# Performance work log

Measured on AMD Instinct MI355X. Metric: run time of the kernel, lower is better.

## Reference

```python
import jax, jax.numpy as jnp
import numpy as np

B, N, M = 2, 2048, 128
H, D = 16, 64
IN_DIM, CTX_DIM = 1024, 768


def layernorm(x, g, b, eps=1e-5):
    mu = x.mean(-1, keepdims=True)
    var = ((x - mu) ** 2).mean(-1, keepdims=True)
    return (x - mu) * jax.lax.rsqrt(var + eps) * g + b


def setup_inputs() -> dict:
    key = jax.random.key(0)
    ks = jax.random.split(key, 8)
    w = lambda i, sh: jax.random.normal(ks[i], sh, jnp.float32) * 0.02
    return {
        "x": jax.random.normal(ks[0], (B, N, IN_DIM), jnp.float32),
        "c_emb": jax.random.normal(ks[1], (B, M, CTX_DIM), jnp.float32),
        "ln_g": jnp.ones((IN_DIM,), jnp.float32),
        "ln_b": jnp.zeros((IN_DIM,), jnp.float32),
        "ctx_ln_g": jnp.ones((CTX_DIM,), jnp.float32),
        "ctx_ln_b": jnp.zeros((CTX_DIM,), jnp.float32),
        "W_ctx": w(2, (CTX_DIM, 2 * D)),
        "b_ctx": jnp.zeros((2 * D,), jnp.float32),
        "W_q": w(3, (IN_DIM, H * D)),
        "W_kv": w(4, (IN_DIM, 2 * H * D)),
        "null_kv": jax.random.normal(ks[5], (2, D), jnp.float32),
        "W_out": w(6, (H * D, IN_DIM)),
        "out_ln_g": jnp.ones((IN_DIM,), jnp.float32),
        "out_ln_b": jnp.zeros((IN_DIM,), jnp.float32),
    }


def reference(x, c_emb, ln_g, ln_b, ctx_ln_g, ctx_ln_b, W_ctx, b_ctx,
              W_q, W_kv, null_kv, W_out, out_ln_g, out_ln_b):
    b, n, _ = x.shape
    xn = layernorm(x, ln_g, ln_b)
    q = (xn @ W_q).reshape(b, n, H, D)                      # [b,n,h,d]
    kv = (xn @ W_kv).reshape(b, n, 2, H, D)
    k, v = kv[:, :, 0], kv[:, :, 1]                         # [b,n,h,d]
    # context projected to a single shared-across-heads k and v
    ckv = layernorm(c_emb, ctx_ln_g, ctx_ln_b) @ W_ctx + b_ctx
    ck, cv = jnp.split(ckv, 2, axis=-1)                     # [b,m,d]
    nk = jnp.broadcast_to(null_kv[0], (b, 1, D))
    nv = jnp.broadcast_to(null_kv[1], (b, 1, D))
    k_ext = jnp.concatenate([nk, ck], axis=1)               # [b,m+1,d]
    v_ext = jnp.concatenate([nv, cv], axis=1)
    scale = D ** -0.5
    s_self = jnp.einsum('bnhd,bkhd->bhnk', q, k) * scale    # [b,h,n,n]
    s_ctx = jnp.einsum('bnhd,bkd->bhnk', q, k_ext) * scale  # [b,h,n,m+1]
    w = jax.nn.softmax(jnp.concatenate([s_self, s_ctx], axis=-1), axis=-1)
    w_self, w_ctx = w[..., :n], w[..., n:]
    out = (jnp.einsum('bhnk,bkhd->bnhd', w_self, v)
           + jnp.einsum('bhnk,bkd->bnhd', w_ctx, v_ext))    # [b,n,h,d]
    out = out.reshape(b, n, H * D) @ W_out                  # [b,n,input_dim]
    return layernorm(out, out_ln_g, out_ln_b)
```

## Files before the change

kernel.cpp:

```cpp
#include <hip/hip_runtime.h>
#include <cstdint>
#include <cstddef>

typedef __attribute__((ext_vector_type(8))) short bf16x8;
typedef __attribute__((ext_vector_type(4))) short bf16x4;
typedef __attribute__((ext_vector_type(4))) float f32x4;
typedef __attribute__((ext_vector_type(4))) unsigned int u32x4;
typedef __attribute__((ext_vector_type(2))) unsigned int u32x2;

__device__ inline unsigned short f2b(float f){
  unsigned int u = __float_as_uint(f);
  u += 0x7fffu + ((u >> 16) & 1u);
  return (unsigned short)(u >> 16);
}
__device__ inline unsigned int pk2(float a, float b){
  unsigned int ua = __float_as_uint(a) + 0x8000u;
  unsigned int ub = __float_as_uint(b) + 0x8000u;
  return __builtin_amdgcn_perm(ub, ua, 0x07060302u);
}
__device__ inline void gl2lds16(const void* g, void* l){
  __builtin_amdgcn_global_load_lds(
      (const __attribute__((address_space(1))) unsigned int*)g,
      (__attribute__((address_space(3))) unsigned int*)l, 16, 0, 0);
}

#define QSCALE 0.18033688011112042f

__global__ __launch_bounds__(256) void wcvt_kernel(
    const float* __restrict__ Wq, const float* __restrict__ Wkv,
    const float* __restrict__ Wout,
    unsigned short* __restrict__ Wqkv_t, unsigned short* __restrict__ Wout_t)
{
  __shared__ short tile[64*72];
  int cg0 = blockIdx.x * 64;
  int kt  = blockIdx.y * 64;
  const float* src; int ld; int col0; unsigned short* dst; int drow0;
  if (cg0 < 1024)      { src = Wq;   ld = 1024; col0 = cg0;        dst = Wqkv_t; drow0 = cg0; }
  else if (cg0 < 3072) { src = Wkv;  ld = 2048; col0 = cg0 - 1024; dst = Wqkv_t; drow0 = cg0; }
  else                 { src = Wout; ld = 1024; col0 = cg0 - 3072; dst = Wout_t; drow0 = cg0 - 3072; }
  int t = threadIdx.x;
  #pragma unroll
  for (int i = 0; i < 16; ++i){
    int lin = t + 256*i;
    int k = lin >> 6, c = lin & 63;
    tile[k*72 + c] = (short)f2b(src[(size_t)(kt + k)*ld + col0 + c]);
  }
  __syncthreads();
  #pragma unroll
  for (int i = 0; i < 16; ++i){
    int lin = t + 256*i;
    int c = lin >> 6, k = lin & 63;
    dst[(size_t)(drow0 + c)*1024 + kt + k] = (unsigned short)tile[k*72 + c];
  }
}

template<bool BF16OUT>
__global__ __launch_bounds__(256) void ln1024_kernel(
    const float* __restrict__ X, const float* __restrict__ G,
    const float* __restrict__ Bb, void* __restrict__ out)
{
  int row = blockIdx.x, t = threadIdx.x;
  float4 x = ((const float4*)(X + (size_t)row*1024))[t];
  float s  = x.x + x.y + x.z + x.w;
  float s2 = x.x*x.x + x.y*x.y + x.z*x.z + x.w*x.w;
  #pragma unroll
  for (int o = 32; o > 0; o >>= 1){ s += __shfl_down(s, o); s2 += __shfl_down(s2, o); }
  __shared__ float red[8];
  int w = t >> 6;
  if ((t & 63) == 0){ red[w] = s; red[4 + w] = s2; }
  __syncthreads();
  float mu  = (red[0]+red[1]+red[2]+red[3]) * (1.0f/1024.0f);
  float var = (red[4]+red[5]+red[6]+red[7]) * (1.0f/1024.0f) - mu*mu;
  float rstd = rsqrtf(var + 1e-5f);
  float4 g = ((const float4*)G)[t];
  float4 b = ((const float4*)Bb)[t];
  float y0 = (x.x-mu)*rstd*g.x + b.x;
  float y1 = (x.y-mu)*rstd*g.y + b.y;
  float y2 = (x.z-mu)*rstd*g.z + b.z;
  float y3 = (x.w-mu)*rstd*g.w + b.w;
  if (BF16OUT){
    ushort4 u; u.x = f2b(y0); u.y = f2b(y1); u.z = f2b(y2); u.w = f2b(y3);
    ((ushort4*)out)[(size_t)row*256 + t] = u;
  } else {
    float4 y; y.x = y0; y.y = y1; y.z = y2; y.w = y3;
    ((float4*)out)[(size_t)row*256 + t] = y;
  }
}

__global__ __launch_bounds__(128) void ctx_kernel(
    const float* __restrict__ Cemb, const float* __restrict__ G,
    const float* __restrict__ Bb, const float* __restrict__ Wctx,
    const float* __restrict__ bctx, const float* __restrict__ nullkv,
    unsigned short* __restrict__ kext, unsigned short* __restrict__ vext_t)
{
  int row = blockIdx.x;
  int b = row >> 7, m = row & 127;
  int t = threadIdx.x;
  if (row < 128){
    int b2 = row >> 6, fr = row & 63;
    int frow = (fr == 0) ? 0 : (128 + fr);
    if (t < 64){
      kext[((size_t)b2*192 + frow)*64 + t] = (frow == 0) ? f2b(nullkv[t]) : (unsigned short)0;
    } else {
      int d = t - 64;
      vext_t[((size_t)b2*64 + d)*192 + frow] = (frow == 0) ? f2b(nullkv[64 + d]) : (unsigned short)0;
    }
  }
  const float* xr = Cemb + (size_t)row*768;
  float v[6]; float s = 0.f, s2 = 0.f;
  #pragma unroll
  for (int j = 0; j < 6; ++j){ float xv = xr[t + 128*j]; v[j] = xv; s += xv; s2 += xv*xv; }
  #pragma unroll
  for (int o = 32; o > 0; o >>= 1){ s += __shfl_down(s, o); s2 += __shfl_down(s2, o); }
  __shared__ float red[4];
  __shared__ float xn[768];
  int w = t >> 6;
  if ((t & 63) == 0){ red[w] = s; red[2 + w] = s2; }
  __syncthreads();
  float mu  = (red[0]+red[1]) * (1.0f/768.0f);
  float var = (red[2]+red[3]) * (1.0f/768.0f) - mu*mu;
  float rstd = rsqrtf(var + 1e-5f);
  #pragma unroll
  for (int j = 0; j < 6; ++j){ int c = t + 128*j; xn[c] = (v[j]-mu)*rstd*G[c] + Bb[c]; }
  __syncthreads();
  float acc = bctx[t];
  #pragma unroll 8
  for (int j = 0; j < 768; ++j) acc += xn[j] * Wctx[j*128 + t];
  unsigned short hv = f2b(acc);
  if (t < 64) kext[((size_t)b*192 + 1 + m)*64 + t] = hv;
  else        vext_t[((size_t)b*64 + (t - 64))*192 + 1 + m] = hv;
}

#define GEMM_MAINLOOP(A_, Bt_, tM_, tN_)                                        \
  __shared__ __align__(16) short sA[128*64];                                    \
  __shared__ __align__(16) short sB[128*64];                                    \
  int t = threadIdx.x, w = t >> 6, lane = t & 63;                               \
  int wm = w & 1, wn = w >> 1, lm = lane & 15, q = lane >> 4;                   \
  int grow = lane >> 3;                                                         \
  int gchk = ((lane & 7) ^ grow) << 3;                                          \
  f32x4 acc[4][4] = {};                                                         \
  const unsigned short* Aw = A_ + (size_t)(tM_ + w*32 + grow)*1024 + gchk;      \
  const unsigned short* Bw = Bt_ + (size_t)(tN_ + w*32 + grow)*1024 + gchk;     \
  for (int kk = 0; kk < 1024; kk += 64){                                        \
    __syncthreads();                                                            \
    gl2lds16(Aw + kk,            &sA[(w*32     )*64]);                          \
    gl2lds16(Aw + kk +  8*1024,  &sA[(w*32 +  8)*64]);                          \
    gl2lds16(Aw + kk + 16*1024,  &sA[(w*32 + 16)*64]);                          \
    gl2lds16(Aw + kk + 24*1024,  &sA[(w*32 + 24)*64]);                          \
    gl2lds16(Bw + kk,            &sB[(w*32     )*64]);                          \
    gl2lds16(Bw + kk +  8*1024,  &sB[(w*32 +  8)*64]);                          \
    gl2lds16(Bw + kk + 16*1024,  &sB[(w*32 + 16)*64]);                          \
    gl2lds16(Bw + kk + 24*1024,  &sB[(w*32 + 24)*64]);                          \
    __syncthreads();                                                            \
    bf16x8 af[4][2], bfr[4][2];                                                 \
    _Pragma("unroll")                                                           \
    for (int i = 0; i < 4; ++i){                                                \
      int ra = wm*64 + i*16 + lm, rb = wn*64 + i*16 + lm;                       \
      _Pragma("unroll")                                                         \
      for (int hh = 0; hh < 2; ++hh){                                           \
        int sw = ((hh*4 + q) ^ (lm & 7)) << 3;                                  \
        af[i][hh]  = *(const bf16x8*)(&sA[ra*64 + sw]);                         \
        bfr[i][hh] = *(const bf16x8*)(&sB[rb*64 + sw]);                         \
      }                                                                         \
    }                                                                           \
    _Pragma("unroll")                                                           \
    for (int hh = 0; hh < 2; ++hh)                                              \
      _Pragma("unroll")                                                         \
      for (int i = 0; i < 4; ++i)                                               \
        _Pragma("unroll")                                                       \
        for (int j = 0; j < 4; ++j)                                             \
          acc[i][j] = __builtin_amdgcn_mfma_f32_16x16x32_bf16(af[i][hh], bfr[j][hh], acc[i][j], 0, 0, 0); \
  }

__global__ __launch_bounds__(256) void gemm_qkv_kernel(
    const unsigned short* __restrict__ A, const unsigned short* __restrict__ Bt,
    unsigned short* __restrict__ Qb, unsigned short* __restrict__ Kb,
    unsigned short* __restrict__ VtG)
{
  int id = blockIdx.x;
  int xcd = id & 7, r = id >> 3;
  int tM = ((r & 3)*8 + xcd) * 128;
  int tN = (r >> 2) * 128;
  GEMM_MAINLOOP(A, Bt, tM, tN)
  if (tN < 1024){
    #pragma unroll
    for (int i = 0; i < 4; ++i){
      int R0 = tM + wm*64 + i*16 + q*4;
      int b = R0 >> 11, n = R0 & 2047;
      #pragma unroll
      for (int j = 0; j < 4; ++j){
        int Cg = tN + wn*64 + j*16 + lm;
        int h = Cg >> 6, d = Cg & 63;
        size_t base = ((((size_t)(b*16 + h) << 11) | n) << 6) + d;
        #pragma unroll
        for (int rr = 0; rr < 4; ++rr)
          Qb[base + (size_t)rr*64] = f2b(acc[i][j][rr] * QSCALE);
      }
    }
  } else if (tN < 2048){
    #pragma unroll
    for (int i = 0; i < 4; ++i){
      int R0 = tM + wm*64 + i*16 + q*4;
      int b = R0 >> 11, n = R0 & 2047;
      #pragma unroll
      for (int j = 0; j < 4; ++j){
        int c2 = tN - 1024 + wn*64 + j*16 + lm;
        int h = c2 >> 6, d = c2 & 63;
        size_t base = ((((size_t)(b*16 + h) << 11) | n) << 6) + d;
        #pragma unroll
        for (int rr = 0; rr < 4; ++rr)
          Kb[base + (size_t)rr*64] = f2b(acc[i][j][rr]);
      }
    }
  } else {
    #pragma unroll
    for (int i = 0; i < 4; ++i){
      int R0 = tM + wm*64 + i*16 + q*4;
      int b = R0 >> 11, n = R0 & 2047;
      #pragma unroll
      for (int j = 0; j < 4; ++j){
        int c2 = tN - 2048 + wn*64 + j*16 + lm;
        int h = c2 >> 6, d = c2 & 63;
        ushort4 u;
        u.x = f2b(acc[i][j][0]); u.y = f2b(acc[i][j][1]);
        u.z = f2b(acc[i][j][2]); u.w = f2b(acc[i][j][3]);
        *(ushort4*)(VtG + ((size_t)(b*16 + h)*64 + d)*2048 + n) = u;
      }
    }
  }
}

__global__ __launch_bounds__(256) void gemm_out_kernel(
    const unsigned short* __restrict__ A, const unsigned short* __restrict__ Bt,
    float* __restrict__ C)
{
  int id = blockIdx.x;
  int xcd = id & 7, r = id >> 3;
  int tM = ((r & 3)*8 + xcd) * 128;
  int tN = (r >> 2) * 128;
  GEMM_MAINLOOP(A, Bt, tM, tN)
  #pragma unroll
  for (int i = 0; i < 4; ++i){
    int R0 = tM + wm*64 + i*16 + q*4;
    #pragma unroll
    for (int j = 0; j < 4; ++j){
      int Cg = tN + wn*64 + j*16 + lm;
      #pragma unroll
      for (int rr = 0; rr < 4; ++rr)
        C[(size_t)(R0 + rr)*1024 + Cg] = acc[i][j][rr];
    }
  }
}

__global__ __launch_bounds__(512, 2) void attn_kernel(
    const unsigned short* __restrict__ Qb, const unsigned short* __restrict__ Kb,
    const unsigned short* __restrict__ VtG, const unsigned short* __restrict__ kext,
    const unsigned short* __restrict__ vext_t, unsigned short* __restrict__ Ob)
{
  __shared__ __align__(16) char smem[81920];
  int id = blockIdx.x;
  int xcd = id & 7, slot = id >> 3;
  int bh = xcd*4 + (slot >> 4);
  int qt = slot & 15;
  int b = bh >> 4, h = bh & 15;
  int t = threadIdx.x, w = t >> 6, lane = t & 63;
  int p = w >> 1, lw = w & 1;
  int lm = lane & 15, q = lane >> 4;
  int esw = lm & 7;

  short* myK = (short*)(smem + p*8192);
  short* myV = (short*)(smem + 32768 + p*8192);
  short* pw  = (short*)(smem + 65536 + w*2048);

  const unsigned short* Qbase = Qb + ((size_t)bh*2048 + qt*128 + lw*64)*64;
  bf16x8 qf[4][2];
  #pragma unroll
  for (int qq = 0; qq < 4; ++qq){
    qf[qq][0] = *(const bf16x8*)(Qbase + (size_t)(qq*16 + lm)*64 + q*8);
    qf[qq][1] = *(const bf16x8*)(Qbase + (size_t)(qq*16 + lm)*64 + q*8 + 32);
  }

  f32x4 o[4][4] = {};
  float l_i[4] = {0.f, 0.f, 0.f, 0.f};

  int pt = t & 127;
  int r0 = pt >> 1, c0 = (pt & 1) << 5;
  int rsw = r0 & 7;
  const int t0 = p*9;
  const int t1 = (p == 3) ? 35 : (t0 + 9);

  u32x4 kr[4], vr[4];
  {
    const unsigned short* kp = Kb + ((size_t)bh*2048 + t0*64 + r0)*64 + c0;
    const unsigned short* vp = VtG + ((size_t)bh*64 + r0)*2048 + t0*64 + c0;
    #pragma unroll
    for (int jj = 0; jj < 4; ++jj){
      kr[jj] = *(const u32x4*)(kp + 8*jj);
      vr[jj] = *(const u32x4*)(vp + 8*jj);
    }
  }

  for (int it = 0; it < 9; ++it){
    int tile = t0 + it;
    bool valid = tile < t1;
    __syncthreads();
    if (valid){
      #pragma unroll
      for (int jj = 0; jj < 4; ++jj){
        int gsw = ((((pt & 1) << 2) | jj) ^ rsw) << 3;
        *(u32x4*)(&myK[r0*64 + gsw]) = kr[jj];
        *(u32x4*)(&myV[r0*64 + gsw]) = vr[jj];
      }
    }
    __syncthreads();

    int nt = tile + 1;
    if (nt < t1){
      bool ext = nt >= 32;
      int kb = ext ? (nt - 32)*64 : nt*64;
      const unsigned short* kp = ext ? (kext + ((size_t)b*192 + kb + r0)*64 + c0)
                                     : (Kb + ((size_t)bh*2048 + kb + r0)*64 + c0);
      const unsigned short* vp = ext ? (vext_t + ((size_t)b*64 + r0)*192 + kb + c0)
                                     : (VtG + ((size_t)bh*64 + r0)*2048 + kb + c0);
      #pragma unroll
      for (int jj = 0; jj < 4; ++jj){
        kr[jj] = *(const u32x4*)(kp + 8*jj);
        vr[jj] = *(const u32x4*)(vp + 8*jj);
      }
    }
    if (!valid) continue;

    bf16x8 kf[4][2];
    #pragma unroll
    for (int st = 0; st < 4; ++st){
      kf[st][0] = *(const bf16x8*)(&myK[(st*16 + lm)*64 + ((q       ^ esw) << 3)]);
      kf[st][1] = *(const bf16x8*)(&myK[(st*16 + lm)*64 + (((4 + q) ^ esw) << 3)]);
    }

    #pragma unroll
    for (int qp = 0; qp < 2; ++qp){
      f32x4 s[2][4];
      #pragma unroll
      for (int qh = 0; qh < 2; ++qh){
        int qq = qp*2 + qh;
        #pragma unroll
        for (int st = 0; st < 4; ++st){
          f32x4 z = {};
          z = __builtin_amdgcn_mfma_f32_16x16x32_bf16(kf[st][0], qf[qq][0], z, 0, 0, 0);
          s[qh][st] = __builtin_amdgcn_mfma_f32_16x16x32_bf16(kf[st][1], qf[qq][1], z, 0, 0, 0);
        }
      }
      if (tile == 34){
        #pragma unroll
        for (int qh = 0; qh < 2; ++qh)
          #pragma unroll
          for (int st = 0; st < 4; ++st)
            #pragma unroll
            for (int rr = 0; rr < 4; ++rr){
              int key = 128 + st*16 + q*4 + rr;
              if (key >= 129) s[qh][st][rr] = -1e30f;
            }
      }
      bf16x8 pb[2][2];
      #pragma unroll
      for (int qh = 0; qh < 2; ++qh){
        float sm = 0.f;
        #pragma unroll
        for (int st = 0; st < 4; ++st)
          #pragma unroll
          for (int rr = 0; rr < 4; ++rr){
            float pv = __builtin_amdgcn_exp2f(s[qh][st][rr]);
            s[qh][st][rr] = pv; sm += pv;
          }
        l_i[qp*2 + qh] += sm;
        #pragma unroll
        for (int st = 0; st < 4; ++st){
          u32x2 pkd;
          pkd[0] = pk2(s[qh][st][0], s[qh][st][1]);
          pkd[1] = pk2(s[qh][st][2], s[qh][st][3]);
          int gsw = ((((st << 1) | (q >> 1)) ^ esw) << 3) + ((q & 1) << 2);
          *(u32x2*)(&pw[lm*64 + gsw]) = pkd;
        }
        bf16x4 a0 = *(const bf16x4*)(&pw[lm*64 + ((q       ^ esw) << 3)]);
        bf16x4 a1 = *(const bf16x4*)(&pw[lm*64 + ((q       ^ esw) << 3) + 4]);
        bf16x4 a2 = *(const bf16x4*)(&pw[lm*64 + (((4 + q) ^ esw) << 3)]);
        bf16x4 a3 = *(const bf16x4*)(&pw[lm*64 + (((4 + q) ^ esw) << 3) + 4]);
        pb[qh][0] = __builtin_shufflevector(a0, a1, 0,1,2,3,4,5,6,7);
        pb[qh][1] = __builtin_shufflevector(a2, a3, 0,1,2,3,4,5,6,7);
      }
      #pragma unroll
      for (int ds = 0; ds < 4; ++ds){
        bf16x8 af0 = *(const bf16x8*)(&myV[(ds*16 + lm)*64 + ((q       ^ esw) << 3)]);
        bf16x8 af1 = *(const bf16x8*)(&myV[(ds*16 + lm)*64 + (((4 + q) ^ esw) << 3)]);
        #pragma unroll
        for (int qh = 0; qh < 2; ++qh){
          int qq = qp*2 + qh;
          o[ds][qq] = __builtin_amdgcn_mfma_f32_16x16x32_bf16(af0, pb[qh][0], o[ds][qq], 0, 0, 0);
          o[ds][qq] = __builtin_amdgcn_mfma_f32_16x16x32_bf16(af1, pb[qh][1], o[ds][qq], 0, 0, 0);
        }
      }
    }
  }

  float* mb = (float*)smem;
  float* lb = (float*)(smem + 65536);
  int ms = ((p >> 1) << 1) | lw;
  float* reg = mb + ms*4096 + lane*64;
  float* lr  = lb + ms*256 + lane*4;
  int fsw = lane & 15;
  __syncthreads();
  if (p & 1){
    #pragma unroll
    for (int ds = 0; ds < 4; ++ds)
      #pragma unroll
      for (int qq = 0; qq < 4; ++qq)
        *(f32x4*)(reg + (((ds*4 + qq) ^ fsw) << 2)) = o[ds][qq];
    #pragma unroll
    for (int qq = 0; qq < 4; ++qq) lr[qq] = l_i[qq];
  }
  __syncthreads();
  if (!(p & 1)){
    #pragma unroll
    for (int ds = 0; ds < 4; ++ds)
      #pragma unroll
      for (int qq = 0; qq < 4; ++qq)
        o[ds][qq] += *(const f32x4*)(reg + (((ds*4 + qq) ^ fsw) << 2));
    #pragma unroll
    for (int qq = 0; qq < 4; ++qq) l_i[qq] += lr[qq];
    if (p == 2){
      #pragma unroll
      for (int ds = 0; ds < 4; ++ds)
        #pragma unroll
        for (int qq = 0; qq < 4; ++qq)
          *(f32x4*)(reg + (((ds*4 + qq) ^ fsw) << 2)) = o[ds][qq];
      #pragma unroll
      for (int qq = 0; qq < 4; ++qq) lr[qq] = l_i[qq];
    }
  }
  __syncthreads();
  if (p == 0){
    float* reg2 = mb + (2 | lw)*4096 + lane*64;
    float* lr2  = lb + (2 | lw)*256 + lane*4;
    #pragma unroll
    for (int qq = 0; qq < 4; ++qq){
      #pragma unroll
      for (int ds = 0; ds < 4; ++ds){
        f32x4 ov = *(const f32x4*)(reg2 + (((ds*4 + qq) ^ fsw) << 2));
        o[ds][qq] += ov;
      }
      float l = l_i[qq] + lr2[qq];
      l += __shfl_xor(l, 16);
      l += __shfl_xor(l, 32);
      float inv = 1.0f / l;
      int n = qt*128 + lw*64 + qq*16 + lm;
      size_t base = ((size_t)b*2048 + n)*1024 + h*64 + q*4;
      #pragma unroll
      for (int ds = 0; ds < 4; ++ds){
        ushort4 u;
        u.x = f2b(o[ds][qq][0] * inv); u.y = f2b(o[ds][qq][1] * inv);
        u.z = f2b(o[ds][qq][2] * inv); u.w = f2b(o[ds][qq][3] * inv);
        *(ushort4*)(Ob + base + ds*16) = u;
      }
    }
  }
}

extern "C" void kernel_launch(void* const* d_in, const int* in_sizes, int n_in,
                              void* d_out, int out_size, void* d_ws, size_t ws_size,
                              hipStream_t stream)
{
  const float* x       = (const float*)d_in[0];
  const float* c_emb   = (const float*)d_in[1];
  const float* ln_g    = (const float*)d_in[2];
  const float* ln_b    = (const float*)d_in[3];
  const float* ctx_g   = (const float*)d_in[4];
  const float* ctx_b   = (const float*)d_in[5];
  const float* W_ctx   = (const float*)d_in[6];
  const float* b_ctx   = (const float*)d_in[7];
  const float* W_q     = (const float*)d_in[8];
  const float* W_kv    = (const float*)d_in[9];
  const float* null_kv = (const float*)d_in[10];
  const float* W_out   = (const float*)d_in[11];
  const float* oln_g   = (const float*)d_in[12];
  const float* oln_b   = (const float*)d_in[13];
  float* out = (float*)d_out;

  char* p = (char*)d_ws;
  unsigned short* xn     = (unsigned short*)p; p += (size_t)4096*1024*2;
  unsigned short* Wqkv_t = (unsigned short*)p; p += (size_t)3072*1024*2;
  unsigned short* Wout_t = (unsigned short*)p; p += (size_t)1024*1024*2;
  unsigned short* Qb     = (unsigned short*)p; p += (size_t)32*2048*64*2;
  unsigned short* Kb     = (unsigned short*)p; p += (size_t)32*2048*64*2;
  unsigned short* VtG    = (unsigned short*)p; p += (size_t)32*64*2048*2;
  unsigned short* kext   = (unsigned short*)p; p += (size_t)2*192*64*2;
  unsigned short* vext_t = (unsigned short*)p; p += (size_t)2*64*192*2;
  unsigned short* aout   = (unsigned short*)p; p += (size_t)4096*1024*2;
  float*          ptmp   = (float*)p;          p += (size_t)4096*1024*4;

  wcvt_kernel<<<dim3(64,16), 256, 0, stream>>>(W_q, W_kv, W_out, Wqkv_t, Wout_t);
  ln1024_kernel<true><<<4096, 256, 0, stream>>>(x, ln_g, ln_b, (void*)xn);
  ctx_kernel<<<256, 128, 0, stream>>>(c_emb, ctx_g, ctx_b, W_ctx, b_ctx, null_kv, kext, vext_t);
  gemm_qkv_kernel<<<768, 256, 0, stream>>>(xn, Wqkv_t, Qb, Kb, VtG);
  attn_kernel<<<512, 512, 0, stream>>>(Qb, Kb, VtG, kext, vext_t, aout);
  gemm_out_kernel<<<256, 256, 0, stream>>>(aout, Wout_t, ptmp);
  ln1024_kernel<false><<<4096, 256, 0, stream>>>(ptmp, oln_g, oln_b, (void*)out);
}
```

Before: 275.9 us.

## Load K/V fragments directly from global memory in attention, drop LDS staging

The attention kernel no longer stages K and V tiles through shared memory with register prefetch and barriers. Each wave now reads its MFMA operand fragments straight from global memory, relying on the caches. Blocks shrink from 512 to 256 threads, each handling 64 queries, with twice as many blocks and less shared memory per block. This removes the per-tile barriers and LDS copies but adds uncached-pattern global loads and duplicates K/V reads across more blocks.

```diff
diff --git a/kernel.cpp b/kernel.cpp
--- a/kernel.cpp
+++ b/kernel.cpp
@@ -252,27 +252,24 @@
   }
 }
 
-__global__ __launch_bounds__(512, 2) void attn_kernel(
+__global__ __launch_bounds__(256, 4) void attn_kernel(
     const unsigned short* __restrict__ Qb, const unsigned short* __restrict__ Kb,
     const unsigned short* __restrict__ VtG, const unsigned short* __restrict__ kext,
     const unsigned short* __restrict__ vext_t, unsigned short* __restrict__ Ob)
 {
-  __shared__ __align__(16) char smem[81920];
+  __shared__ __align__(16) char smem[36864];
   int id = blockIdx.x;
-  int xcd = id & 7, slot = id >> 3;
-  int bh = xcd*4 + (slot >> 4);
-  int qt = slot & 15;
+  int xcd = id & 7, s = id >> 3;
+  int bh = xcd*4 + (s >> 5);
+  int q64 = s & 31;
   int b = bh >> 4, h = bh & 15;
   int t = threadIdx.x, w = t >> 6, lane = t & 63;
-  int p = w >> 1, lw = w & 1;
   int lm = lane & 15, q = lane >> 4;
   int esw = lm & 7;
 
-  short* myK = (short*)(smem + p*8192);
-  short* myV = (short*)(smem + 32768 + p*8192);
-  short* pw  = (short*)(smem + 65536 + w*2048);
-
-  const unsigned short* Qbase = Qb + ((size_t)bh*2048 + qt*128 + lw*64)*64;
+  short* pw = (short*)(smem + w*2048);
+
+  const unsigned short* Qbase = Qb + ((size_t)bh*2048 + q64*64)*64;
   bf16x8 qf[4][2];
   #pragma unroll
   for (int qq = 0; qq < 4; ++qq){
@@ -283,63 +280,29 @@
   f32x4 o[4][4] = {};
   float l_i[4] = {0.f, 0.f, 0.f, 0.f};
 
-  int pt = t & 127;
-  int r0 = pt >> 1, c0 = (pt & 1) << 5;
-  int rsw = r0 & 7;
-  const int t0 = p*9;
-  const int t1 = (p == 3) ? 35 : (t0 + 9);
-
-  u32x4 kr[4], vr[4];
-  {
-    const unsigned short* kp = Kb + ((size_t)bh*2048 + t0*64 + r0)*64 + c0;
-    const unsigned short* vp = VtG + ((size_t)bh*64 + r0)*2048 + t0*64 + c0;
-    #pragma unroll
-    for (int jj = 0; jj < 4; ++jj){
-      kr[jj] = *(const u32x4*)(kp + 8*jj);
-      vr[jj] = *(const u32x4*)(vp + 8*jj);
-    }
-  }
-
-  for (int it = 0; it < 9; ++it){
-    int tile = t0 + it;
-    bool valid = tile < t1;
-    __syncthreads();
-    if (valid){
-      #pragma unroll
-      for (int jj = 0; jj < 4; ++jj){
-        int gsw = ((((pt & 1) << 2) | jj) ^ rsw) << 3;
-        *(u32x4*)(&myK[r0*64 + gsw]) = kr[jj];
-        *(u32x4*)(&myV[r0*64 + gsw]) = vr[jj];
-      }
-    }
-    __syncthreads();
-
-    int nt = tile + 1;
-    if (nt < t1){
-      bool ext = nt >= 32;
-      int kb = ext ? (nt - 32)*64 : nt*64;
-      const unsigned short* kp = ext ? (kext + ((size_t)b*192 + kb + r0)*64 + c0)
-                                     : (Kb + ((size_t)bh*2048 + kb + r0)*64 + c0);
-      const unsigned short* vp = ext ? (vext_t + ((size_t)b*64 + r0)*192 + kb + c0)
-                                     : (VtG + ((size_t)bh*64 + r0)*2048 + kb + c0);
-      #pragma unroll
-      for (int jj = 0; jj < 4; ++jj){
-        kr[jj] = *(const u32x4*)(kp + 8*jj);
-        vr[jj] = *(const u32x4*)(vp + 8*jj);
-      }
-    }
-    if (!valid) continue;
-
+  const int t0 = w*9;
+  const int t1 = (w == 3) ? 35 : (t0 + 9);
+
+  for (int tile = t0; tile < t1; ++tile){
+    bool ext = tile >= 32;
+    const unsigned short* kp = ext
+        ? kext + ((size_t)b*192 + (tile - 32)*64)*64
+        : Kb   + ((size_t)bh*2048 + tile*64)*64;
     bf16x8 kf[4][2];
     #pragma unroll
     for (int st = 0; st < 4; ++st){
-      kf[st][0] = *(const bf16x8*)(&myK[(st*16 + lm)*64 + ((q       ^ esw) << 3)]);
-      kf[st][1] = *(const bf16x8*)(&myK[(st*16 + lm)*64 + (((4 + q) ^ esw) << 3)]);
-    }
+      const unsigned short* kr = kp + (size_t)(st*16 + lm)*64 + q*8;
+      kf[st][0] = *(const bf16x8*)(kr);
+      kf[st][1] = *(const bf16x8*)(kr + 32);
+    }
+    const unsigned short* vp = ext
+        ? vext_t + (size_t)b*64*192 + (tile - 32)*64
+        : VtG    + (size_t)bh*64*2048 + tile*64;
+    size_t vstride = ext ? 192 : 2048;
 
     #pragma unroll
     for (int qp = 0; qp < 2; ++qp){
-      f32x4 s[2][4];
+      f32x4 sc[2][4];
       #pragma unroll
       for (int qh = 0; qh < 2; ++qh){
         int qq = qp*2 + qh;
@@ -347,7 +310,7 @@
         for (int st = 0; st < 4; ++st){
           f32x4 z = {};
           z = __builtin_amdgcn_mfma_f32_16x16x32_bf16(kf[st][0], qf[qq][0], z, 0, 0, 0);
-          s[qh][st] = __builtin_amdgcn_mfma_f32_16x16x32_bf16(kf[st][1], qf[qq][1], z, 0, 0, 0);
+          sc[qh][st] = __builtin_amdgcn_mfma_f32_16x16x32_bf16(kf[st][1], qf[qq][1], z, 0, 0, 0);
         }
       }
       if (tile == 34){
@@ -358,7 +321,7 @@
             #pragma unroll
             for (int rr = 0; rr < 4; ++rr){
               int key = 128 + st*16 + q*4 + rr;
-              if (key >= 129) s[qh][st][rr] = -1e30f;
+              if (key >= 129) sc[qh][st][rr] = -1e30f;
             }
       }
       bf16x8 pb[2][2];
@@ -369,15 +332,15 @@
         for (int st = 0; st < 4; ++st)
           #pragma unroll
           for (int rr = 0; rr < 4; ++rr){
-            float pv = __builtin_amdgcn_exp2f(s[qh][st][rr]);
-            s[qh][st][rr] = pv; sm += pv;
+            float pv = __builtin_amdgcn_exp2f(sc[qh][st][rr]);
+            sc[qh][st][rr] = pv; sm += pv;
           }
         l_i[qp*2 + qh] += sm;
         #pragma unroll
         for (int st = 0; st < 4; ++st){
           u32x2 pkd;
-          pkd[0] = pk2(s[qh][st][0], s[qh][st][1]);
-          pkd[1] = pk2(s[qh][st][2], s[qh][st][3]);
+          pkd[0] = pk2(sc[qh][st][0], sc[qh][st][1]);
+          pkd[1] = pk2(sc[qh][st][2], sc[qh][st][3]);
           int gsw = ((((st << 1) | (q >> 1)) ^ esw) << 3) + ((q & 1) << 2);
           *(u32x2*)(&pw[lm*64 + gsw]) = pkd;
         }
@@ -390,8 +353,9 @@
       }
       #pragma unroll
       for (int ds = 0; ds < 4; ++ds){
-        bf16x8 af0 = *(const bf16x8*)(&myV[(ds*16 + lm)*64 + ((q       ^ esw) << 3)]);
-        bf16x8 af1 = *(const bf16x8*)(&myV[(ds*16 + lm)*64 + (((4 + q) ^ esw) << 3)]);
+        const unsigned short* vr = vp + (size_t)(ds*16 + lm)*vstride + q*8;
+        bf16x8 af0 = *(const bf16x8*)(vr);
+        bf16x8 af1 = *(const bf16x8*)(vr + 32);
         #pragma unroll
         for (int qh = 0; qh < 2; ++qh){
           int qq = qp*2 + qh;
@@ -403,13 +367,12 @@
   }
 
   float* mb = (float*)smem;
-  float* lb = (float*)(smem + 65536);
-  int ms = ((p >> 1) << 1) | lw;
-  float* reg = mb + ms*4096 + lane*64;
-  float* lr  = lb + ms*256 + lane*4;
+  float* lb = (float*)(smem + 32768);
+  float* reg = mb + (w >> 1)*4096 + lane*64;
+  float* lr  = lb + (w >> 1)*256 + lane*4;
   int fsw = lane & 15;
   __syncthreads();
-  if (p & 1){
+  if (w & 1){
     #pragma unroll
     for (int ds = 0; ds < 4; ++ds)
       #pragma unroll
@@ -419,7 +382,7 @@
     for (int qq = 0; qq < 4; ++qq) lr[qq] = l_i[qq];
   }
   __syncthreads();
-  if (!(p & 1)){
+  if (!(w & 1)){
     #pragma unroll
     for (int ds = 0; ds < 4; ++ds)
       #pragma unroll
@@ -427,7 +390,7 @@
         o[ds][qq] += *(const f32x4*)(reg + (((ds*4 + qq) ^ fsw) << 2));
     #pragma unroll
     for (int qq = 0; qq < 4; ++qq) l_i[qq] += lr[qq];
-    if (p == 2){
+    if (w == 2){
       #pragma unroll
       for (int ds = 0; ds < 4; ++ds)
         #pragma unroll
@@ -438,9 +401,9 @@
     }
   }
   __syncthreads();
-  if (p == 0){
-    float* reg2 = mb + (2 | lw)*4096 + lane*64;
-    float* lr2  = lb + (2 | lw)*256 + lane*4;
+  if (w == 0){
+    float* reg2 = mb + 4096 + lane*64;
+    float* lr2  = lb + 256 + lane*4;
     #pragma unroll
     for (int qq = 0; qq < 4; ++qq){
       #pragma unroll
@@ -452,7 +415,7 @@
       l += __shfl_xor(l, 16);
       l += __shfl_xor(l, 32);
       float inv = 1.0f / l;
-      int n = qt*128 + lw*64 + qq*16 + lm;
+      int n = q64*64 + qq*16 + lm;
       size_t base = ((size_t)b*2048 + n)*1024 + h*64 + q*4;
       #pragma unroll
       for (int ds = 0; ds < 4; ++ds){
@@ -501,7 +464,7 @@
   ln1024_kernel<true><<<4096, 256, 0, stream>>>(x, ln_g, ln_b, (void*)xn);
   ctx_kernel<<<256, 128, 0, stream>>>(c_emb, ctx_g, ctx_b, W_ctx, b_ctx, null_kv, kext, vext_t);
   gemm_qkv_kernel<<<768, 256, 0, stream>>>(xn, Wqkv_t, Qb, Kb, VtG);
-  attn_kernel<<<512, 512, 0, stream>>>(Qb, Kb, VtG, kext, vext_t, aout);
+  attn_kernel<<<1024, 256, 0, stream>>>(Qb, Kb, VtG, kext, vext_t, aout);
   gemm_out_kernel<<<256, 256, 0, stream>>>(aout, Wout_t, ptmp);
   ln1024_kernel<false><<<4096, 256, 0, stream>>>(ptmp, oln_g, oln_b, (void*)out);
 }
```

After: 497.8 us. +80.4%, slower.
